# Performance work log

Measured on AMD Instinct MI355X. Metric: run time of the kernel, lower is better.

Reference implementation:

```python
import jax, jax.numpy as jnp
import numpy as np

B, N, E, H = 16, 768, 1024, 16  # batch == heads so mask[i] (head-indexed, as in the source) is valid
D = E // H
MASK_P = 0.1
NEG = jnp.float32(-1e16)


def setup_inputs() -> dict:
    key = jax.random.key(0)
    ks = jax.random.split(key, 8)
    query = jax.random.normal(ks[0], (B, N, E), jnp.float32)
    key_t = jax.random.normal(ks[1], (B, N, E), jnp.float32)
    value = jax.random.normal(ks[2], (B, N, E), jnp.float32)
    u = jax.random.uniform(ks[3], (B, N))
    mask = jnp.where(u < MASK_P, -jnp.inf, 0.0).astype(jnp.float32)
    # per-head Linear(head_dim, head_dim, bias=False) weights, stacked over heads: (H, out=D, in=D)
    Wq = jax.random.normal(ks[4], (H, D, D), jnp.float32) * (1.0 / np.sqrt(D))
    Wk = jax.random.normal(ks[5], (H, D, D), jnp.float32) * (1.0 / np.sqrt(D))
    Wv = jax.random.normal(ks[6], (H, D, D), jnp.float32) * (1.0 / np.sqrt(D))
    Wf = jax.random.normal(ks[7], (E, E), jnp.float32) * (1.0 / np.sqrt(E))
    return {"query": query, "key": key_t, "value": value, "mask": mask,
            "Wq": Wq, "Wk": Wk, "Wv": Wv, "Wf": Wf}


def reference(query, key, value, mask, Wq, Wk, Wv, Wf):
    b, n, e = query.shape
    h = Wq.shape[0]
    d = e // h
    q = query.reshape(b, n, h, d)
    k = key.reshape(b, n, h, d)
    v = value.reshape(b, n, h, d)
    # per-head nn.Linear: x @ W[i].T  (W: (H, out, in))
    qh = jnp.einsum('bnhd,hed->bnhe', q, Wq)
    kh = jnp.einsum('bnhd,hed->bnhe', k, Wk)
    vh = jnp.einsum('bnhd,hed->bnhe', v, Wv)
    # scaled QK^T: divide by embed_size**0.5 (NOT head_dim) as in the source
    scores = jnp.einsum('bqhd,bkhd->bhqk', qh, kh) / jnp.sqrt(jnp.float32(e))  # (B,H,N,N)
    # faithful quirk: mask row selected by HEAD index i -> same additive mask for all batches
    bad = jnp.isneginf(mask)[:h]                      # (H, N)
    add = jnp.where(bad[:, :, None] | bad[:, None, :], NEG, jnp.float32(0.0))  # (H,N,N): row/col blanked
    probs = jax.nn.softmax(scores + add[None], axis=-1)
    attn = jnp.einsum('bhqk,bkhd->bqhd', probs, vh)   # (B,N,H,D)
    out = attn.reshape(b, n, e) @ Wf.T
    return out
```

## Files before the change

kernel.cpp:

```cpp
#include <hip/hip_runtime.h>

#define B_ 16
#define N_ 768
#define E_ 1024
#define H_ 16
#define D_ 64

typedef __bf16 bf16x8 __attribute__((ext_vector_type(8)));
typedef float f32x4 __attribute__((ext_vector_type(4)));
typedef unsigned short ushort8 __attribute__((ext_vector_type(8)));
typedef unsigned short ushort4v __attribute__((ext_vector_type(4)));
typedef unsigned int uint2v __attribute__((ext_vector_type(2)));
typedef unsigned int uint4v __attribute__((ext_vector_type(4)));

__device__ __forceinline__ unsigned short f2bf(float x) {
  unsigned u = __builtin_bit_cast(unsigned, x);
  u += 0x7FFFu + ((u >> 16) & 1u);
  return (unsigned short)(u >> 16);
}

__device__ __forceinline__ unsigned cvtpk(float lo, float hi) {
  unsigned r;
  asm("v_cvt_pk_bf16_f32 %0, %1, %2" : "=v"(r) : "v"(lo), "v"(hi));
  return r;
}

__device__ __forceinline__ f32x4 mfma16(ushort8 a, ushort8 b, f32x4 c) {
  return __builtin_amdgcn_mfma_f32_16x16x32_bf16(
      __builtin_bit_cast(bf16x8, a), __builtin_bit_cast(bf16x8, b), c, 0, 0, 0);
}

__global__ __launch_bounds__(256) void proj_kernel(
    const float* __restrict__ q, const float* __restrict__ k, const float* __restrict__ v,
    const float* __restrict__ Wq, const float* __restrict__ Wk, const float* __restrict__ Wv,
    const float* __restrict__ Wf, unsigned short* __restrict__ Qh,
    unsigned short* __restrict__ Kh, unsigned short* __restrict__ Vt,
    unsigned short* __restrict__ Wfb) {
  const int nt = blockIdx.x % 12;
  const int bh = blockIdx.x / 12;
  const int b = bh >> 4, h = bh & 15;
  const int tid = threadIdx.x;
  const int w = tid >> 6, l = tid & 63;
  const int l16 = l & 15, lg = l >> 4;

  if (blockIdx.x < 1024) {
    size_t g = (size_t)blockIdx.x * 256 + tid;
    float4 xv = *(const float4*)&Wf[g * 4];
    ushort4v s;
    s[0] = f2bf(xv.x); s[1] = f2bf(xv.y); s[2] = f2bf(xv.z); s[3] = f2bf(xv.w);
    *(ushort4v*)&Wfb[g * 4] = s;
  }

  __shared__ __align__(16) unsigned short Xs[3][64][72];
  __shared__ __align__(16) unsigned short Ws[3][64][72];

  const float* xin[3] = {q, k, v};
  const float* win[3] = {Wq, Wk, Wv};

#pragma unroll
  for (int m = 0; m < 3; ++m) {
    const float* xp = xin[m];
#pragma unroll
    for (int i = 0; i < 4; ++i) {
      int flat = i * 256 + tid;
      int row = flat >> 4;
      int c4 = (flat & 15) * 4;
      float4 xv = *(const float4*)&xp[((size_t)(b * N_ + nt * 64 + row)) * E_ + h * 64 + c4];
      ushort4v s;
      s[0] = f2bf(xv.x); s[1] = f2bf(xv.y); s[2] = f2bf(xv.z); s[3] = f2bf(xv.w);
      *(ushort4v*)&Xs[m][row][c4] = s;
    }
    const float* wp = win[m] + (size_t)h * 4096;
#pragma unroll
    for (int i = 0; i < 4; ++i) {
      int flat = i * 256 + tid;
      int row = flat >> 4;
      int c4 = (flat & 15) * 4;
      float4 wv = *(const float4*)&wp[row * 64 + c4];
      ushort4v s;
      s[0] = f2bf(wv.x); s[1] = f2bf(wv.y); s[2] = f2bf(wv.z); s[3] = f2bf(wv.w);
      *(ushort4v*)&Ws[m][row][c4] = s;
    }
  }
  __syncthreads();

  f32x4 vacc[4];
#pragma unroll
  for (int m = 0; m < 3; ++m) {
    f32x4 acc[4] = {};
#pragma unroll
    for (int kc = 0; kc < 2; ++kc) {
      ushort8 a = *(const ushort8*)&Xs[m][w * 16 + l16][kc * 32 + lg * 8];
#pragma unroll
      for (int eg = 0; eg < 4; ++eg) {
        ushort8 bf = *(const ushort8*)&Ws[m][eg * 16 + l16][kc * 32 + lg * 8];
        acc[eg] = mfma16(a, bf, acc[eg]);
      }
    }
    if (m == 2) {
#pragma unroll
      for (int eg = 0; eg < 4; ++eg) vacc[eg] = acc[eg];
    } else {
      unsigned short* op = (m == 0) ? Qh : Kh;
#pragma unroll
      for (int eg = 0; eg < 4; ++eg)
#pragma unroll
        for (int r = 0; r < 4; ++r)
          op[((size_t)(b * H_ + h) * N_ + nt * 64 + w * 16 + lg * 4 + r) * 64 + eg * 16 + l16] =
              f2bf(acc[eg][r]);
    }
  }

  __syncthreads();
#pragma unroll
  for (int eg = 0; eg < 4; ++eg) {
    uint2v pk;
    pk[0] = cvtpk(vacc[eg][0], vacc[eg][1]);
    pk[1] = cvtpk(vacc[eg][2], vacc[eg][3]);
    *(uint2v*)&Xs[0][eg * 16 + l16][w * 16 + lg * 4] = pk;
  }
  __syncthreads();
#pragma unroll
  for (int i = 0; i < 2; ++i) {
    int row = i * 32 + (tid >> 3), c8 = (tid & 7) * 8;
    *(ushort8*)&Vt[((size_t)bh * 64 + row) * N_ + nt * 64 + c8] =
        *(const ushort8*)&Xs[0][row][c8];
  }
}

__global__ __launch_bounds__(256, 4) void attn_kernel(
    const unsigned short* __restrict__ Qh, const unsigned short* __restrict__ Kh,
    const unsigned short* __restrict__ Vt, const float* __restrict__ mask,
    unsigned short* __restrict__ attnO) {
  const int bid = blockIdx.x;
  const int logical = (bid & 7) * 192 + (bid >> 3);
  const int qt = logical % 6;
  const int bh = logical / 6;
  const int b = bh >> 4, h = bh & 15;
  const int tid = threadIdx.x;
  const int w = tid >> 6, l = tid & 63;
  const int l16 = l & 15, lg = l >> 4;

  __shared__ __align__(16) unsigned short Ks[64][72];
  __shared__ __align__(16) unsigned short Vs[64][72];
  __shared__ __align__(16) unsigned short Ps[4][32][72];
  __shared__ float badk[N_];

  const size_t baseK = (size_t)bh * N_ * 64;
  const size_t baseV = (size_t)bh * 64 * N_;
  const int qrow0 = qt * 128 + w * 32;

  for (int i = tid; i < N_; i += 256) badk[i] = (mask[h * N_ + i] < -1e30f) ? 1.f : 0.f;

  ushort8 bQ[2][2];
#pragma unroll
  for (int qs = 0; qs < 2; ++qs)
#pragma unroll
    for (int kc = 0; kc < 2; ++kc)
      bQ[qs][kc] = *(const ushort8*)&Qh[((size_t)bh * N_ + qrow0 + qs * 16 + l16) * 64 +
                                        kc * 32 + lg * 8];
  float bqf[2];
#pragma unroll
  for (int qs = 0; qs < 2; ++qs)
    bqf[qs] = (mask[h * N_ + qrow0 + qs * 16 + l16] < -1e30f) ? 1.f : 0.f;

  const int srow = tid >> 3;
  const int sc8 = (tid & 7) * 8;

  uint4v kreg[2], vreg[2];
#pragma unroll
  for (int i = 0; i < 2; ++i) {
    int row = i * 32 + srow;
    kreg[i] = *(const uint4v*)&Kh[baseK + (size_t)row * 64 + sc8];
    vreg[i] = *(const uint4v*)&Vt[baseV + (size_t)row * N_ + sc8];
  }
  __syncthreads();
#pragma unroll
  for (int i = 0; i < 2; ++i) {
    int row = i * 32 + srow;
    *(ushort8*)&Ks[row][sc8] = __builtin_bit_cast(ushort8, kreg[i]);
    *(ushort8*)&Vs[row][sc8] = __builtin_bit_cast(ushort8, vreg[i]);
  }
  __syncthreads();

  f32x4 oacc[2][4] = {};
  float l_part[2] = {0.f, 0.f};

  for (int kt = 0; kt < 12; ++kt) {
    if (kt < 11) {
#pragma unroll
      for (int i = 0; i < 2; ++i) {
        int row = i * 32 + srow;
        kreg[i] = *(const uint4v*)&Kh[baseK + (size_t)((kt + 1) * 64 + row) * 64 + sc8];
        vreg[i] = *(const uint4v*)&Vt[baseV + (size_t)row * N_ + (kt + 1) * 64 + sc8];
      }
    }

#pragma unroll
    for (int cg = 0; cg < 4; ++cg) {
      f32x4 st[2] = {};
#pragma unroll
      for (int kc = 0; kc < 2; ++kc) {
        ushort8 aK = *(const ushort8*)&Ks[cg * 16 + l16][kc * 32 + lg * 8];
        st[0] = mfma16(aK, bQ[0][kc], st[0]);
        st[1] = mfma16(aK, bQ[1][kc], st[1]);
      }
      f32x4 bk4 = *(const f32x4*)&badk[kt * 64 + cg * 16 + lg * 4];
#pragma unroll
      for (int qs = 0; qs < 2; ++qs) {
        float p[4];
#pragma unroll
        for (int r = 0; r < 4; ++r) {
          float t = st[qs][r] * 0.03125f;
          t = (bk4[r] > 0.f) ? -1e16f : t;
          t = (bqf[qs] > 0.f) ? 0.f : t;
          p[r] = __expf(t);
          l_part[qs] += p[r];
        }
        uint2v pk;
        pk[0] = cvtpk(p[0], p[1]);
        pk[1] = cvtpk(p[2], p[3]);
        *(uint2v*)&Ps[w][qs * 16 + l16][cg * 16 + lg * 4] = pk;
      }
    }

#pragma unroll
    for (int kc = 0; kc < 2; ++kc) {
      ushort8 ap[2];
#pragma unroll
      for (int qs = 0; qs < 2; ++qs)
        ap[qs] = *(const ushort8*)&Ps[w][qs * 16 + l16][kc * 32 + lg * 8];
#pragma unroll
      for (int dg = 0; dg < 4; ++dg) {
        ushort8 bv = *(const ushort8*)&Vs[dg * 16 + l16][kc * 32 + lg * 8];
        oacc[0][dg] = mfma16(ap[0], bv, oacc[0][dg]);
        oacc[1][dg] = mfma16(ap[1], bv, oacc[1][dg]);
      }
    }

    __syncthreads();
    if (kt < 11) {
#pragma unroll
      for (int i = 0; i < 2; ++i) {
        int row = i * 32 + srow;
        *(ushort8*)&Ks[row][sc8] = __builtin_bit_cast(ushort8, kreg[i]);
        *(ushort8*)&Vs[row][sc8] = __builtin_bit_cast(ushort8, vreg[i]);
      }
    }
    __syncthreads();
  }

#pragma unroll
  for (int qs = 0; qs < 2; ++qs) {
    float s = l_part[qs];
    s += __shfl_xor(s, 16);
    s += __shfl_xor(s, 32);
#pragma unroll
    for (int r = 0; r < 4; ++r) {
      float dnm = __shfl(s, lg * 4 + r);
      float inv = 1.f / dnm;
      int qg = qrow0 + qs * 16 + lg * 4 + r;
      size_t orow = ((size_t)b * N_ + qg) * E_ + h * 64;
#pragma unroll
      for (int dg = 0; dg < 4; ++dg)
        attnO[orow + dg * 16 + l16] = f2bf(oacc[qs][dg][r] * inv);
    }
  }
}

__global__ __launch_bounds__(256) void gemm_kernel(const unsigned short* __restrict__ A,
                                                   const unsigned short* __restrict__ Bm,
                                                   float* __restrict__ out) {
  const int be = blockIdx.x & 7;
  const int bm = blockIdx.x >> 3;
  const int tid = threadIdx.x;
  const int w = tid >> 6, l = tid & 63;
  const int l16 = l & 15, lg = l >> 4;
  const int wm = w >> 1, wn = w & 1;

  __shared__ __align__(16) unsigned short As[128][72];
  __shared__ __align__(16) unsigned short Bs[128][72];

  f32x4 acc[4][4] = {};
  const int m0 = bm * 128, e0 = be * 128;
  const int srow = tid >> 3, sc8 = (tid & 7) * 8;
  const unsigned short* Ab = A + (size_t)(m0 + srow) * E_ + sc8;
  const unsigned short* Bb = Bm + (size_t)(e0 + srow) * E_ + sc8;

  uint4v ar[4], br[4];
#pragma unroll
  for (int i = 0; i < 4; ++i) {
    ar[i] = *(const uint4v*)(Ab + (size_t)i * 32 * E_);
    br[i] = *(const uint4v*)(Bb + (size_t)i * 32 * E_);
  }

  for (int kk = 0; kk < 16; ++kk) {
    __syncthreads();
#pragma unroll
    for (int i = 0; i < 4; ++i) {
      *(ushort8*)&As[i * 32 + srow][sc8] = __builtin_bit_cast(ushort8, ar[i]);
      *(ushort8*)&Bs[i * 32 + srow][sc8] = __builtin_bit_cast(ushort8, br[i]);
    }
    __syncthreads();
    if (kk < 15) {
#pragma unroll
      for (int i = 0; i < 4; ++i) {
        ar[i] = *(const uint4v*)(Ab + (size_t)i * 32 * E_ + (kk + 1) * 64);
        br[i] = *(const uint4v*)(Bb + (size_t)i * 32 * E_ + (kk + 1) * 64);
      }
    }
#pragma unroll
    for (int kc = 0; kc < 2; ++kc) {
      ushort8 a[4], bf[4];
#pragma unroll
      for (int i = 0; i < 4; ++i)
        a[i] = *(const ushort8*)&As[wm * 64 + i * 16 + l16][kc * 32 + lg * 8];
#pragma unroll
      for (int j = 0; j < 4; ++j)
        bf[j] = *(const ushort8*)&Bs[wn * 64 + j * 16 + l16][kc * 32 + lg * 8];
#pragma unroll
      for (int i = 0; i < 4; ++i)
#pragma unroll
        for (int j = 0; j < 4; ++j) acc[i][j] = mfma16(a[i], bf[j], acc[i][j]);
    }
  }

#pragma unroll
  for (int i = 0; i < 4; ++i)
#pragma unroll
    for (int j = 0; j < 4; ++j)
#pragma unroll
      for (int r = 0; r < 4; ++r)
        out[(size_t)(m0 + wm * 64 + i * 16 + lg * 4 + r) * E_ + e0 + wn * 64 + j * 16 + l16] =
            acc[i][j][r];
}

extern "C" void kernel_launch(void* const* d_in, const int* in_sizes, int n_in,
                              void* d_out, int out_size, void* d_ws, size_t ws_size,
                              hipStream_t stream) {
  const float* q = (const float*)d_in[0];
  const float* k = (const float*)d_in[1];
  const float* v = (const float*)d_in[2];
  const float* mask = (const float*)d_in[3];
  const float* Wq = (const float*)d_in[4];
  const float* Wk = (const float*)d_in[5];
  const float* Wv = (const float*)d_in[6];
  const float* Wf = (const float*)d_in[7];
  float* out = (float*)d_out;

  const size_t PH = (size_t)B_ * H_ * N_ * D_;
  unsigned short* Qh = (unsigned short*)d_ws;
  unsigned short* Kh = Qh + PH;
  unsigned short* Vt = Kh + PH;
  unsigned short* attn = Vt + PH;
  unsigned short* Wfb = attn + PH;

  proj_kernel<<<B_ * H_ * (N_ / 64), 256, 0, stream>>>(q, k, v, Wq, Wk, Wv, Wf, Qh, Kh, Vt,
                                                       Wfb);
  attn_kernel<<<B_ * H_ * (N_ / 128), 256, 0, stream>>>(Qh, Kh, Vt, mask, attn);
  gemm_kernel<<<(B_ * N_ / 128) * (E_ / 128), 256, 0, stream>>>(attn, Wfb, out);
}
```

Before: 153.5 us.

## Use exp2 with folded additive mask in attention; direct global-to-LDS loads in GEMM

In the attention kernel, the score scale and log2(e) are folded into a single FMA with an additive mask bias, and raw v_exp_f32 (exp2) replaces __expf, which drops two selects and one multiply per element. In the output GEMM, the register-staged prefetch is replaced by global_load_lds DMA straight into unpadded LDS tiles, followed by a full vmcnt wait each iteration. This cuts VGPR use and LDS store instructions, but it loses the overlap between next-tile loads and compute. The unpadded 64-element row stride may also cause LDS bank conflicts on the MFMA operand reads.

```diff
diff --git a/kernel.cpp b/kernel.cpp
--- a/kernel.cpp
+++ b/kernel.cpp
@@ -25,10 +25,21 @@
   return r;
 }
 
+__device__ __forceinline__ float fexp2(float x) {
+  float r;
+  asm("v_exp_f32 %0, %1" : "=v"(r) : "v"(x));
+  return r;
+}
+
 __device__ __forceinline__ f32x4 mfma16(ushort8 a, ushort8 b, f32x4 c) {
   return __builtin_amdgcn_mfma_f32_16x16x32_bf16(
       __builtin_bit_cast(bf16x8, a), __builtin_bit_cast(bf16x8, b), c, 0, 0, 0);
 }
+
+#define GLD16(gsrc, ldst)                                              \
+  __builtin_amdgcn_global_load_lds(                                   \
+      (const __attribute__((address_space(1))) void*)(gsrc),          \
+      (__attribute__((address_space(3))) void*)(ldst), 16, 0, 0)
 
 __global__ __launch_bounds__(256) void proj_kernel(
     const float* __restrict__ q, const float* __restrict__ k, const float* __restrict__ v,
@@ -144,13 +155,15 @@
   __shared__ __align__(16) unsigned short Ks[64][72];
   __shared__ __align__(16) unsigned short Vs[64][72];
   __shared__ __align__(16) unsigned short Ps[4][32][72];
-  __shared__ float badk[N_];
+  __shared__ float addk[N_];
 
   const size_t baseK = (size_t)bh * N_ * 64;
   const size_t baseV = (size_t)bh * 64 * N_;
   const int qrow0 = qt * 128 + w * 32;
-
-  for (int i = tid; i < N_; i += 256) badk[i] = (mask[h * N_ + i] < -1e30f) ? 1.f : 0.f;
+  const float C2 = 0.04508422f;
+
+  for (int i = tid; i < N_; i += 256)
+    addk[i] = (mask[h * N_ + i] < -1e30f) ? -1.0e20f : 0.0f;
 
   ushort8 bQ[2][2];
 #pragma unroll
@@ -205,16 +218,15 @@
         st[0] = mfma16(aK, bQ[0][kc], st[0]);
         st[1] = mfma16(aK, bQ[1][kc], st[1]);
       }
-      f32x4 bk4 = *(const f32x4*)&badk[kt * 64 + cg * 16 + lg * 4];
+      f32x4 ak4 = *(const f32x4*)&addk[kt * 64 + cg * 16 + lg * 4];
 #pragma unroll
       for (int qs = 0; qs < 2; ++qs) {
         float p[4];
 #pragma unroll
         for (int r = 0; r < 4; ++r) {
-          float t = st[qs][r] * 0.03125f;
-          t = (bk4[r] > 0.f) ? -1e16f : t;
-          t = (bqf[qs] > 0.f) ? 0.f : t;
-          p[r] = __expf(t);
+          float t = __builtin_fmaf(st[qs][r], C2, ak4[r]);
+          t = (bqf[qs] > 0.f) ? 0.0f : t;
+          p[r] = fexp2(t);
           l_part[qs] += p[r];
         }
         uint2v pk;
@@ -278,46 +290,44 @@
   const int l16 = l & 15, lg = l >> 4;
   const int wm = w >> 1, wn = w & 1;
 
-  __shared__ __align__(16) unsigned short As[128][72];
-  __shared__ __align__(16) unsigned short Bs[128][72];
+  __shared__ __align__(16) unsigned short As[128 * 64];
+  __shared__ __align__(16) unsigned short Bs[128 * 64];
+
+  const int m0 = bm * 128, e0 = be * 128;
+
+  const int srow8 = l >> 3;
+  const int scol = (l & 7) * 8;
+  const unsigned short* gA[4];
+  const unsigned short* gB[4];
+#pragma unroll
+  for (int j = 0; j < 4; ++j) {
+    int tr = (w * 4 + j) * 8 + srow8;
+    gA[j] = A + (size_t)(m0 + tr) * E_ + scol;
+    gB[j] = Bm + (size_t)(e0 + tr) * E_ + scol;
+  }
 
   f32x4 acc[4][4] = {};
-  const int m0 = bm * 128, e0 = be * 128;
-  const int srow = tid >> 3, sc8 = (tid & 7) * 8;
-  const unsigned short* Ab = A + (size_t)(m0 + srow) * E_ + sc8;
-  const unsigned short* Bb = Bm + (size_t)(e0 + srow) * E_ + sc8;
-
-  uint4v ar[4], br[4];
-#pragma unroll
-  for (int i = 0; i < 4; ++i) {
-    ar[i] = *(const uint4v*)(Ab + (size_t)i * 32 * E_);
-    br[i] = *(const uint4v*)(Bb + (size_t)i * 32 * E_);
-  }
 
   for (int kk = 0; kk < 16; ++kk) {
     __syncthreads();
 #pragma unroll
-    for (int i = 0; i < 4; ++i) {
-      *(ushort8*)&As[i * 32 + srow][sc8] = __builtin_bit_cast(ushort8, ar[i]);
-      *(ushort8*)&Bs[i * 32 + srow][sc8] = __builtin_bit_cast(ushort8, br[i]);
-    }
+    for (int j = 0; j < 4; ++j) {
+      int ch = w * 4 + j;
+      GLD16(gA[j] + kk * 64, (char*)As + ch * 1024);
+      GLD16(gB[j] + kk * 64, (char*)Bs + ch * 1024);
+    }
+    asm volatile("s_waitcnt vmcnt(0)" ::: "memory");
     __syncthreads();
-    if (kk < 15) {
-#pragma unroll
-      for (int i = 0; i < 4; ++i) {
-        ar[i] = *(const uint4v*)(Ab + (size_t)i * 32 * E_ + (kk + 1) * 64);
-        br[i] = *(const uint4v*)(Bb + (size_t)i * 32 * E_ + (kk + 1) * 64);
-      }
-    }
+
 #pragma unroll
     for (int kc = 0; kc < 2; ++kc) {
       ushort8 a[4], bf[4];
 #pragma unroll
       for (int i = 0; i < 4; ++i)
-        a[i] = *(const ushort8*)&As[wm * 64 + i * 16 + l16][kc * 32 + lg * 8];
+        a[i] = *(const ushort8*)&As[(wm * 64 + i * 16 + l16) * 64 + kc * 32 + lg * 8];
 #pragma unroll
       for (int j = 0; j < 4; ++j)
-        bf[j] = *(const ushort8*)&Bs[wn * 64 + j * 16 + l16][kc * 32 + lg * 8];
+        bf[j] = *(const ushort8*)&Bs[(wn * 64 + j * 16 + l16) * 64 + kc * 32 + lg * 8];
 #pragma unroll
       for (int i = 0; i < 4; ++i)
 #pragma unroll
```

After: 161.8 us. +5.4%, slower.
